# Performance work log

Measured on AMD Instinct MI355X. Metric: run time of the kernel, lower is better.

## Reference

```python
import jax, jax.numpy as jnp
import numpy as np

COND_EPS = 1e-12  # singularity threshold for the 2x2 Hessian determinant


def setup_inputs() -> dict:
    key = jax.random.key(0)
    k1, k2 = jax.random.split(key)
    b, h, w = 8, 1024, 1536
    # neur_beta_eme: non-negative-ish network output (forward clamps at 0 anyway)
    neur_beta_eme = jax.random.uniform(k1, (b, 1, h, w), dtype=jnp.float32) * 2.0
    base_detector_score = jax.random.normal(k2, (b, 1, h, w), dtype=jnp.float32)
    return {
        "neur_beta_eme": neur_beta_eme,
        "base_detector_score": base_detector_score,
        "n": 2048,
        "border_size": 16,
    }


def _gather(score_flat, y, x, w):
    # score_flat: [b, h*w]; y,x: [b,n] -> [b,n]
    return jnp.take_along_axis(score_flat, y * w + x, axis=-1)


def reference(neur_beta_eme, base_detector_score, n, border_size):
    b, _, h, w = base_detector_score.shape
    # NeSSDetector.forward: model(image)[-1].clamp(min=0)
    neur = jnp.maximum(neur_beta_eme, 0.0)
    score = base_detector_score

    # base_detector.get_extrema_mask: 3x3 NMS (local max) + border exclusion
    pooled = jax.lax.reduce_window(score, -jnp.inf, jax.lax.max,
                                   (1, 1, 3, 3), (1, 1, 1, 1), "SAME")
    ys = jnp.arange(h)
    xs = jnp.arange(w)
    border = (((ys >= border_size) & (ys < h - border_size))[:, None]
              & ((xs >= border_size) & (xs < w - border_size))[None, :])
    extrema_mask = (score == pooled) & border[None, None]

    # ness_extrema_map = exp(-neur_beta_eme) * extrema_mask
    ness = jnp.exp(-neur) * extrema_mask.astype(score.dtype)

    # topk over flattened spatial dims
    ness_flat = ness.reshape(b, -1)                      # [b, h*w]
    _, flat_cand_kp = jax.lax.top_k(ness_flat, n)        # [b, n]

    # flat2grid(flat, w) + 0.5  (pixel-center coords, (y, x) order)
    y = flat_cand_kp // w
    x = flat_cand_kp % w
    cand_kp = jnp.stack([y, x], axis=-1).astype(score.dtype) + 0.5  # [b, n, 2]

    # localize_keypoints_via_taylor: 3x3 finite-difference gradient/Hessian,
    # solve H @ inc = -g per keypoint (2x2 closed-form solve)
    sf = score.reshape(b, -1)
    yc = jnp.clip(y, 1, h - 2)
    xc = jnp.clip(x, 1, w - 2)
    s00 = _gather(sf, yc, xc, w)
    sp0 = _gather(sf, yc + 1, xc, w)
    sm0 = _gather(sf, yc - 1, xc, w)
    s0p = _gather(sf, yc, xc + 1, w)
    s0m = _gather(sf, yc, xc - 1, w)
    spp = _gather(sf, yc + 1, xc + 1, w)
    spm = _gather(sf, yc + 1, xc - 1, w)
    smp = _gather(sf, yc - 1, xc + 1, w)
    smm = _gather(sf, yc - 1, xc - 1, w)

    gy = 0.5 * (sp0 - sm0)
    gx = 0.5 * (s0p - s0m)
    hyy = sp0 - 2.0 * s00 + sm0
    hxx = s0p - 2.0 * s00 + s0m
    hxy = 0.25 * (spp - spm - smp + smm)

    det = hyy * hxx - hxy * hxy
    sing_mask = jnp.abs(det) > COND_EPS
    safe_det = jnp.where(sing_mask, det, 1.0)
    inc_y = -(hxx * gy - hxy * gx) / safe_det
    inc_x = -(hyy * gx - hxy * gy) / safe_det
    inc = jnp.stack([inc_y, inc_x], axis=-1)             # [b, n, 2]
    inc = jnp.clip(jnp.where(sing_mask[..., None], inc, 0.0), -0.5, 0.5)

    kp = cand_kp + inc                                   # [b, n, 2]

    # kp_neur_beta_eme = neur.view(b,-1).gather(-1, flat_cand_kp)
    kp_neur = jnp.take_along_axis(neur.reshape(b, -1), flat_cand_kp, axis=-1)

    return jnp.concatenate([kp, kp_neur[..., None]], axis=-1)  # [b, n, 3]
```

## Files before the change

### kernel.cpp

```cpp
#include <hip/hip_runtime.h>
#include <math.h>

typedef unsigned int u32;
typedef unsigned long long u64;

#define B 8
#define H 1024
#define W 1536
#define NPIX (H * W)
#define NK 2048
#define BORDER 16
#define NSEG 64
#define TY 8
#define NTILE 6
#define GRIDY 31
#define HBINS 512
#define TOPK_CAP 4096
#define SEG_CAP_MAX 4096
#define CTR_PAD 32
#define IDX_MASK 0x1FFFFFu

#define OFF_TCOUNT 128
#define OFF_HIST   4096
#define OFF_SEGCNT 20480
#define OFF_ZERO_END 86016
#define OFF_KEYS   86016
#define OFF_CAND   348160

__global__ __launch_bounds__(256) void cand_k(const float* __restrict__ neur,
                                              const float* __restrict__ score,
                                              u32* __restrict__ candp,
                                              u32* __restrict__ segcnt,
                                              u32* __restrict__ hist, int seg_cap) {
    __shared__ u32 lh[HBINS];
    int tile = blockIdx.x;
    int b = blockIdx.z;
    int wave = threadIdx.x >> 6;
    int lane = threadIdx.x & 63;
    for (int i = threadIdx.x; i < HBINS; i += 256) lh[i] = 0;
    __syncthreads();

    int strip = blockIdx.y * 4 + wave;
    int y0 = BORDER + strip * TY;
    int x0 = tile * 256 + lane * 4;
    const float* s = score + (size_t)b * NPIX;
    const float* nb = neur + (size_t)b * NPIX;
    bool haveL = (tile > 0) && (lane == 0);
    bool haveR = (tile < NTILE - 1) && (lane == 63);

    float4 rv[TY + 2];
    float4 nvv[TY];
    float le[TY + 2], re[TY + 2];
    const float* base_row = s + (size_t)(y0 - 1) * W + x0;
    const float* nrow = nb + (size_t)y0 * W + x0;
    #pragma unroll
    for (int r = 0; r < TY + 2; ++r) rv[r] = *(const float4*)(base_row + (size_t)r * W);
    #pragma unroll
    for (int r = 0; r < TY; ++r) nvv[r] = *(const float4*)(nrow + (size_t)r * W);
    #pragma unroll
    for (int r = 0; r < TY + 2; ++r) {
        le[r] = haveL ? base_row[(size_t)r * W - 1] : 0.0f;
        re[r] = haveR ? base_row[(size_t)r * W + 4] : 0.0f;
    }

    bool xok[4];
    #pragma unroll
    for (int e = 0; e < 4; ++e) {
        int x = x0 + e;
        xok[e] = (x >= BORDER) && (x < W - BORDER);
    }

    u32 extbits = 0;
    {
        float4 hm, h0, hp;
        #pragma unroll
        for (int r = 0; r < 2; ++r) {
            float4 c = rv[r];
            float l = __shfl_up(c.w, 1); if (haveL) l = le[r];
            float rr = __shfl_down(c.x, 1); if (haveR) rr = re[r];
            float4 hh;
            hh.x = fmaxf(fmaxf(l, c.x), c.y);
            hh.y = fmaxf(fmaxf(c.x, c.y), c.z);
            hh.z = fmaxf(fmaxf(c.y, c.z), c.w);
            hh.w = fmaxf(fmaxf(c.z, c.w), rr);
            if (r == 0) hm = hh; else h0 = hh;
        }
        #pragma unroll
        for (int ys = 0; ys < TY; ++ys) {
            float4 c = rv[ys + 2];
            float l = __shfl_up(c.w, 1); if (haveL) l = le[ys + 2];
            float rr = __shfl_down(c.x, 1); if (haveR) rr = re[ys + 2];
            hp.x = fmaxf(fmaxf(l, c.x), c.y);
            hp.y = fmaxf(fmaxf(c.x, c.y), c.z);
            hp.z = fmaxf(fmaxf(c.y, c.z), c.w);
            hp.w = fmaxf(fmaxf(c.z, c.w), rr);
            float pv[4];
            pv[0] = fmaxf(fmaxf(hm.x, h0.x), hp.x);
            pv[1] = fmaxf(fmaxf(hm.y, h0.y), hp.y);
            pv[2] = fmaxf(fmaxf(hm.z, h0.z), hp.z);
            pv[3] = fmaxf(fmaxf(hm.w, h0.w), hp.w);
            float4 c0 = rv[ys + 1];
            float cv[4] = {c0.x, c0.y, c0.z, c0.w};
            #pragma unroll
            for (int e = 0; e < 4; ++e)
                if (xok[e] && cv[e] >= pv[e]) extbits |= (1u << (ys * 4 + e));
            hm = h0; h0 = hp;
        }
    }

    u32 c = (u32)__popc(extbits);
    u32 scan = c;
    #pragma unroll
    for (int off = 1; off < 64; off <<= 1) {
        u32 o = (u32)__shfl_up((int)scan, off, 64);
        if (lane >= off) scan += o;
    }
    u32 excl = scan - c;
    u32 tot = (u32)__shfl((int)scan, 63, 64);
    if (tot) {
        int seg = (strip * NTILE + tile) & (NSEG - 1);
        u32* ctr = &segcnt[(u32)(b * NSEG + seg) * CTR_PAD];
        u32 base = 0;
        if (lane == 63) base = atomicAdd(ctr, scan);
        base = (u32)__shfl((int)base, 63, 64);
        u32 pos0 = base + excl;
        u32 sbase = (u32)(b * NSEG + seg) * (u32)seg_cap;
        u32 idxbase = (u32)(y0 * W + x0);
        #pragma unroll
        for (int k = 0; k < 32; ++k) {
            if (extbits & (1u << k)) {
                const int ro = k >> 2, e = k & 3;
                float4 nq = nvv[ro];
                float raw = (e == 0) ? nq.x : (e == 1) ? nq.y : (e == 2) ? nq.z : nq.w;
                float nv = fmaxf(raw, 0.0f);
                u32 fb = __float_as_uint(nv);
                u32 bin = fb >> 21; if (bin > HBINS - 1) bin = HBINS - 1;
                atomicAdd(&lh[bin], 1u);
                u32 idx = idxbase + (u32)ro * W + (u32)e;
                u32 p = pos0 + (u32)__popc(extbits & ((1u << k) - 1u));
                if ((int)p < seg_cap) candp[sbase + p] = (bin << 21) | idx;
            }
        }
    }
    __syncthreads();
    for (int i = threadIdx.x; i < HBINS; i += 256) {
        u32 v = lh[i];
        if (v) atomicAdd(&hist[(u32)b * HBINS + i], v);
    }
}

__global__ __launch_bounds__(256) void compact_k(const u32* __restrict__ candp,
                                                 const u32* __restrict__ segcnt,
                                                 const u32* __restrict__ hist,
                                                 const float* __restrict__ neur,
                                                 u64* __restrict__ keysout,
                                                 u32* tcount, int seg_cap) {
    __shared__ u32 piv_s;
    int seg = blockIdx.x;
    int b = blockIdx.y;
    int lane = threadIdx.x & 63;
    if (threadIdx.x < 64) {
        if (threadIdx.x == 0) piv_s = 0xFFFFFFFFu;
        u32 v[8];
        u32 s8 = 0;
        #pragma unroll
        for (int e = 0; e < 8; ++e) {
            v[e] = hist[(u32)b * HBINS + (u32)threadIdx.x * 8u + e];
            s8 += v[e];
        }
        u32 incl = s8;
        #pragma unroll
        for (int off = 1; off < 64; off <<= 1) {
            u32 o = (u32)__shfl_up((int)incl, off, 64);
            if (lane >= off) incl += o;
        }
        u32 excl = incl - s8;
        if (excl < NK && incl >= NK) {
            u32 cum = excl;
            u32 T = 0;
            #pragma unroll
            for (int e = 0; e < 8; ++e) {
                cum += v[e];
                if (cum >= NK) { T = (u32)threadIdx.x * 8u + e; break; }
            }
            piv_s = (T + 2u) << 21;
        }
    }
    __syncthreads();
    u32 piv = piv_s;
    const float* nb = neur + (size_t)b * NPIX;

    u32 cnt = segcnt[(u32)(b * NSEG + seg) * CTR_PAD];
    if ((int)cnt > seg_cap) cnt = (u32)seg_cap;
    u32 base = (u32)(b * NSEG + seg) * (u32)seg_cap;
    u32 iters = (cnt + 255u) / 256u;
    for (u32 it = 0; it < iters; ++it) {
        u32 i = it * 256u + threadIdx.x;
        bool f = false;
        u32 idx = 0;
        if (i < cnt) {
            u32 p = candp[base + i];
            f = (p < piv);
            idx = p & IDX_MASK;
        }
        u64 m = __ballot((int)f);
        if (m) {
            int leader = __ffsll((long long)m) - 1;
            u32 wbase = 0;
            if (lane == leader) wbase = atomicAdd(&tcount[b * CTR_PAD], (u32)__popcll(m));
            wbase = (u32)__shfl((int)wbase, leader, 64);
            if (f) {
                u32 pos = wbase + (u32)__popcll(m & ((1ull << (u32)lane) - 1ull));
                if (pos < TOPK_CAP) {
                    float nv = fmaxf(nb[idx], 0.0f);
                    float ness = (float)exp(-(double)nv);
                    keysout[(u32)b * TOPK_CAP + pos] =
                        ((u64)__float_as_uint(ness) << 32) | (u32)(~idx);
                }
            }
        }
    }
}

__global__ __launch_bounds__(256, 1) void rankref_k(const float* __restrict__ neur,
                                                    const float* __restrict__ score,
                                                    const u64* __restrict__ keys,
                                                    const u32* __restrict__ tcount,
                                                    float* __restrict__ out) {
    __shared__ u32 part[3][64];
    int b = blockIdx.y;
    int wave = threadIdx.x >> 6;
    int lane = threadIdx.x & 63;
    u32 cnt = tcount[(u32)b * CTR_PAD];
    if (cnt > TOPK_CAP) cnt = TOPK_CAP;
    const u64* kb = keys + (u32)b * TOPK_CAP;

    u32 i = blockIdx.x * 64u + (u32)lane;
    u64 kown = (i < cnt) ? kb[i] : 0ull;

    int rem = (int)cnt - wave * 1024;
    u32 nj = rem <= 0 ? 0u : (rem > 1024 ? 1024u : (u32)rem);
    const u64* kq = kb + (u32)wave * 1024u;

    u32 myrank = 0;
    u32 nj8 = nj & ~7u;
    for (u32 j = 0; j < nj8; j += 8u) {
        #pragma unroll
        for (int e = 0; e < 8; ++e) {
            u64 ki = kq[j + (u32)e];
            myrank += (ki > kown) ? 1u : 0u;
        }
    }
    for (u32 j = nj8; j < nj; ++j) {
        u64 ki = kq[j];
        myrank += (ki > kown) ? 1u : 0u;
    }

    if (wave) part[wave - 1][lane] = myrank;
    __syncthreads();
    if (wave) return;
    myrank += part[0][lane] + part[1][lane] + part[2][lane];

    if (i >= cnt || myrank >= NK) return;

    u32 idx = ~(u32)kown;
    if (idx >= (u32)NPIX) return;
    const float* s = score + (size_t)b * NPIX;
    const float* nb = neur + (size_t)b * NPIX;
    int y = (int)(idx / W), x = (int)(idx % W);
    int yc = min(max(y, 1), H - 2), xc = min(max(x, 1), W - 2);
    int p = yc * W + xc;
    float s00 = s[p], sp0 = s[p + W], sm0 = s[p - W], s0p = s[p + 1], s0m = s[p - 1];
    float spp = s[p + W + 1], spm = s[p + W - 1], smp = s[p - W + 1], smm = s[p - W - 1];
    float gy = 0.5f * (sp0 - sm0);
    float gx = 0.5f * (s0p - s0m);
    float hyy = sp0 - 2.0f * s00 + sm0;
    float hxx = s0p - 2.0f * s00 + s0m;
    float hxy = 0.25f * (spp - spm - smp + smm);
    float det = hyy * hxx - hxy * hxy;
    bool sing = fabsf(det) > 1e-12f;
    float sd = sing ? det : 1.0f;
    float iy = -(hxx * gy - hxy * gx) / sd;
    float ix = -(hyy * gx - hxy * gy) / sd;
    if (!sing) { iy = 0.0f; ix = 0.0f; }
    iy = fminf(fmaxf(iy, -0.5f), 0.5f);
    ix = fminf(fmaxf(ix, -0.5f), 0.5f);
    size_t o = ((size_t)b * NK + (size_t)myrank) * 3;
    out[o] = (float)y + 0.5f + iy;
    out[o + 1] = (float)x + 0.5f + ix;
    out[o + 2] = fmaxf(nb[idx], 0.0f);
}

extern "C" void kernel_launch(void* const* d_in, const int* in_sizes, int n_in,
                              void* d_out, int out_size, void* d_ws, size_t ws_size,
                              hipStream_t stream) {
    const float* neur = (const float*)d_in[0];
    const float* score = (const float*)d_in[1];
    float* out = (float*)d_out;
    char* ws = (char*)d_ws;
    u32* tcount = (u32*)(ws + OFF_TCOUNT);
    u32* hist = (u32*)(ws + OFF_HIST);
    u32* segcnt = (u32*)(ws + OFF_SEGCNT);
    u64* keysbuf = (u64*)(ws + OFF_KEYS);
    u32* candp = (u32*)(ws + OFF_CAND);

    size_t avail = ws_size > OFF_CAND ? ws_size - OFF_CAND : 0;
    long long cap_ll = (long long)(avail / (4ull * B * NSEG));
    int seg_cap = cap_ll > SEG_CAP_MAX ? SEG_CAP_MAX : (int)cap_ll;

    hipMemsetAsync(ws, 0, OFF_ZERO_END, stream);
    cand_k<<<dim3(NTILE, GRIDY, B), 256, 0, stream>>>(neur, score, candp, segcnt, hist, seg_cap);
    compact_k<<<dim3(NSEG, B), 256, 0, stream>>>(candp, segcnt, hist, neur, keysbuf, tcount, seg_cap);
    rankref_k<<<dim3(TOPK_CAP / 64, B), 256, 0, stream>>>(neur, score, keysbuf, tcount, out);
}
```

Measured before the change: 186.2 us.

## Rank keys via scalar-loaded full buffer with 8 waves per block

The rank-by-counting kernel now zeroes the whole key buffer with the memset, so every wave can compare against all TOPK_CAP slots without bounds checks. Keys are read with inline-asm s_load_dwordx16 into scalar registers, and each block runs 512 threads over eight 512-key slices. This removes per-lane vector loads of shared keys and count-dependent loop bounds. In exchange the memset grows to about 340KB, every block does the full 4096 comparisons regardless of the real candidate count, and each scalar load waits on lgkmcnt(0) with no overlap.

```diff
diff --git a/kernel.cpp b/kernel.cpp
--- a/kernel.cpp
+++ b/kernel.cpp
@@ -3,6 +3,7 @@
 
 typedef unsigned int u32;
 typedef unsigned long long u64;
+typedef int v16i __attribute__((ext_vector_type(16)));
 
 #define B 8
 #define H 1024
@@ -23,8 +24,8 @@
 #define OFF_TCOUNT 128
 #define OFF_HIST   4096
 #define OFF_SEGCNT 20480
-#define OFF_ZERO_END 86016
 #define OFF_KEYS   86016
+#define OFF_ZERO_END 348160
 #define OFF_CAND   348160
 
 __global__ __launch_bounds__(256) void cand_k(const float* __restrict__ neur,
@@ -222,12 +223,12 @@
     }
 }
 
-__global__ __launch_bounds__(256, 1) void rankref_k(const float* __restrict__ neur,
+__global__ __launch_bounds__(512, 1) void rankref_k(const float* __restrict__ neur,
                                                     const float* __restrict__ score,
                                                     const u64* __restrict__ keys,
                                                     const u32* __restrict__ tcount,
                                                     float* __restrict__ out) {
-    __shared__ u32 part[3][64];
+    __shared__ u32 part[7][64];
     int b = blockIdx.y;
     int wave = threadIdx.x >> 6;
     int lane = threadIdx.x & 63;
@@ -236,30 +237,46 @@
     const u64* kb = keys + (u32)b * TOPK_CAP;
 
     u32 i = blockIdx.x * 64u + (u32)lane;
-    u64 kown = (i < cnt) ? kb[i] : 0ull;
-
-    int rem = (int)cnt - wave * 1024;
-    u32 nj = rem <= 0 ? 0u : (rem > 1024 ? 1024u : (u32)rem);
-    const u64* kq = kb + (u32)wave * 1024u;
-
-    u32 myrank = 0;
-    u32 nj8 = nj & ~7u;
-    for (u32 j = 0; j < nj8; j += 8u) {
-        #pragma unroll
-        for (int e = 0; e < 8; ++e) {
-            u64 ki = kq[j + (u32)e];
-            myrank += (ki > kown) ? 1u : 0u;
-        }
-    }
-    for (u32 j = nj8; j < nj; ++j) {
-        u64 ki = kq[j];
-        myrank += (ki > kown) ? 1u : 0u;
-    }
+    u64 kown = kb[i];
+
+    u32 jbase = (u32)wave * 512u;
+    uintptr_t p = (uintptr_t)(kb + jbase);
+    u32 plo = (u32)__builtin_amdgcn_readfirstlane((int)(u32)p);
+    u32 phi = (u32)__builtin_amdgcn_readfirstlane((int)(u32)(p >> 32));
+    const u64* kqu = (const u64*)(((uintptr_t)phi << 32) | (uintptr_t)plo);
+
+    u32 r0 = 0, r1 = 0, r2 = 0, r3 = 0;
+    #pragma unroll 2
+    for (int g = 0; g < 64; ++g) {
+        v16i kk;
+        asm volatile("s_load_dwordx16 %0, %1, 0x0\n\ts_waitcnt lgkmcnt(0)"
+                     : "=s"(kk)
+                     : "s"(kqu + (size_t)g * 8)
+                     : "memory");
+        u64 k0 = ((u64)(u32)kk[1]  << 32) | (u64)(u32)kk[0];
+        u64 k1 = ((u64)(u32)kk[3]  << 32) | (u64)(u32)kk[2];
+        u64 k2 = ((u64)(u32)kk[5]  << 32) | (u64)(u32)kk[4];
+        u64 k3 = ((u64)(u32)kk[7]  << 32) | (u64)(u32)kk[6];
+        u64 k4 = ((u64)(u32)kk[9]  << 32) | (u64)(u32)kk[8];
+        u64 k5 = ((u64)(u32)kk[11] << 32) | (u64)(u32)kk[10];
+        u64 k6 = ((u64)(u32)kk[13] << 32) | (u64)(u32)kk[12];
+        u64 k7 = ((u64)(u32)kk[15] << 32) | (u64)(u32)kk[14];
+        r0 += (k0 > kown) ? 1u : 0u;
+        r1 += (k1 > kown) ? 1u : 0u;
+        r2 += (k2 > kown) ? 1u : 0u;
+        r3 += (k3 > kown) ? 1u : 0u;
+        r0 += (k4 > kown) ? 1u : 0u;
+        r1 += (k5 > kown) ? 1u : 0u;
+        r2 += (k6 > kown) ? 1u : 0u;
+        r3 += (k7 > kown) ? 1u : 0u;
+    }
+    u32 myrank = (r0 + r1) + (r2 + r3);
 
     if (wave) part[wave - 1][lane] = myrank;
     __syncthreads();
     if (wave) return;
-    myrank += part[0][lane] + part[1][lane] + part[2][lane];
+    #pragma unroll
+    for (int wv = 0; wv < 7; ++wv) myrank += part[wv][lane];
 
     if (i >= cnt || myrank >= NK) return;
 
@@ -269,9 +286,9 @@
     const float* nb = neur + (size_t)b * NPIX;
     int y = (int)(idx / W), x = (int)(idx % W);
     int yc = min(max(y, 1), H - 2), xc = min(max(x, 1), W - 2);
-    int p = yc * W + xc;
-    float s00 = s[p], sp0 = s[p + W], sm0 = s[p - W], s0p = s[p + 1], s0m = s[p - 1];
-    float spp = s[p + W + 1], spm = s[p + W - 1], smp = s[p - W + 1], smm = s[p - W - 1];
+    int pp = yc * W + xc;
+    float s00 = s[pp], sp0 = s[pp + W], sm0 = s[pp - W], s0p = s[pp + 1], s0m = s[pp - 1];
+    float spp = s[pp + W + 1], spm = s[pp + W - 1], smp = s[pp - W + 1], smm = s[pp - W - 1];
     float gy = 0.5f * (sp0 - sm0);
     float gx = 0.5f * (s0p - s0m);
     float hyy = sp0 - 2.0f * s00 + sm0;
@@ -311,5 +328,5 @@
     hipMemsetAsync(ws, 0, OFF_ZERO_END, stream);
     cand_k<<<dim3(NTILE, GRIDY, B), 256, 0, stream>>>(neur, score, candp, segcnt, hist, seg_cap);
     compact_k<<<dim3(NSEG, B), 256, 0, stream>>>(candp, segcnt, hist, neur, keysbuf, tcount, seg_cap);
-    rankref_k<<<dim3(TOPK_CAP / 64, B), 256, 0, stream>>>(neur, score, keysbuf, tcount, out);
+    rankref_k<<<dim3(TOPK_CAP / 64, B), 512, 0, stream>>>(neur, score, keysbuf, tcount, out);
 }
```

Result: faster. 173.6 us (-6.7%).
